# Optimization experiments

Hardware: AMD Instinct MI355X
Metric: run time of the kernel (lower is better)

## Reference

```python
import jax, jax.numpy as jnp
import numpy as np

N = 50000          # nodes
E = 800000         # directed edges (before self-loops)
F_IN = 256
HIDS = 32
HEADS = 8
N_CLASSES = 40
NEG_SLOPE = 0.2    # PyG GATConv default leaky_relu slope


def setup_inputs() -> dict:
    key = jax.random.key(0)
    ks = jax.random.split(key, 10)
    x = jax.random.normal(ks[0], (N, F_IN), dtype=jnp.float32)
    edge_index = jax.random.randint(ks[1], (2, E), 0, N, dtype=jnp.int32)
    # conv1: F_IN -> HIDS per head, HEADS heads, concat=True
    W1 = jax.random.normal(ks[2], (F_IN, HEADS * HIDS), dtype=jnp.float32) * (1.0 / np.sqrt(F_IN))
    a1_src = jax.random.normal(ks[3], (HEADS, HIDS), dtype=jnp.float32) * 0.1
    a1_dst = jax.random.normal(ks[4], (HEADS, HIDS), dtype=jnp.float32) * 0.1
    b1 = jnp.zeros((HEADS * HIDS,), dtype=jnp.float32)
    # conv2: HEADS*HIDS -> N_CLASSES, 1 head, concat=False
    W2 = jax.random.normal(ks[5], (HEADS * HIDS, N_CLASSES), dtype=jnp.float32) * (1.0 / np.sqrt(HEADS * HIDS))
    a2_src = jax.random.normal(ks[6], (1, N_CLASSES), dtype=jnp.float32) * 0.1
    a2_dst = jax.random.normal(ks[7], (1, N_CLASSES), dtype=jnp.float32) * 0.1
    b2 = jnp.zeros((N_CLASSES,), dtype=jnp.float32)
    return {"x": x, "edge_index": edge_index, "W1": W1, "a1_src": a1_src,
            "a1_dst": a1_dst, "b1": b1, "W2": W2, "a2_src": a2_src,
            "a2_dst": a2_dst, "b2": b2}


def _gat_conv(x, src, dst, W, a_src, a_dst, bias, heads, concat):
    n = x.shape[0]
    c = W.shape[1] // heads
    xw = (x @ W).reshape(n, heads, c)                       # [N,H,C]
    alpha_s = jnp.einsum('nhc,hc->nh', xw, a_src)           # [N,H]
    alpha_d = jnp.einsum('nhc,hc->nh', xw, a_dst)
    e = alpha_s[src] + alpha_d[dst]                         # [Etot,H]
    e = jnp.where(e >= 0, e, NEG_SLOPE * e)                 # leaky_relu
    # segment softmax over incoming edges of each destination node
    m = jax.ops.segment_max(e, dst, num_segments=n)         # [N,H]
    ex = jnp.exp(e - m[dst])
    denom = jax.ops.segment_sum(ex, dst, num_segments=n)    # [N,H]
    alpha = ex / denom[dst]                                 # [Etot,H]
    out = jax.ops.segment_sum(alpha[:, :, None] * xw[src], dst, num_segments=n)  # [N,H,C]
    if concat:
        out = out.reshape(n, heads * c)
    else:
        out = out.mean(axis=1)
    return out + bias


def reference(x, edge_index, W1, a1_src, a1_dst, b1, W2, a2_src, a2_dst, b2):
    n = x.shape[0]
    # add self-loops (PyG GATConv default)
    loop = jnp.arange(n, dtype=edge_index.dtype)
    src = jnp.concatenate([edge_index[0], loop])
    dst = jnp.concatenate([edge_index[1], loop])
    # dropout(p=0.6) layers are identity in eval mode
    h = _gat_conv(x, src, dst, W1, a1_src, a1_dst, b1, HEADS, True)
    h = jax.nn.elu(h)
    out = _gat_conv(h, src, dst, W2, a2_src, a2_dst, b2, 1, False)
    return out
```

## Files before the change

kernel.cpp:

```cpp
#include <hip/hip_runtime.h>
#include <hip/hip_bf16.h>

#define NNODES 50000
#define NPAD   50048
#define NEDGES 800000
#define ETOT   (NEDGES + NNODES)
#define FIN    256
#define HIDS   32
#define HEADS  8
#define NCLS   40
#define NEG    0.2f

#define SCAN_B 256
#define NSCB   ((NNODES + SCAN_B - 1) / SCAN_B)

typedef __attribute__((ext_vector_type(8))) short bf16x8;
typedef __attribute__((ext_vector_type(4))) float f32x4;

__device__ __forceinline__ ushort f2bf(float f) {
  unsigned u = __float_as_uint(f);
  unsigned r = (u + 0x7fffu + ((u >> 16) & 1u)) >> 16;
  return (ushort)r;
}
__device__ __forceinline__ float bf2f(ushort u) {
  return __uint_as_float(((unsigned)u) << 16);
}

__global__ __launch_bounds__(256) void conv_x(const float* __restrict__ x, ushort* __restrict__ xb) {
  size_t gid = (size_t)blockIdx.x * 256 + threadIdx.x;
  int row = (int)(gid >> 5);
  int c0 = ((int)gid & 31) * 8;
  if (row >= NPAD) return;
  bf16x8 o;
  if (row < NNODES) {
    const float4* xp = (const float4*)(x + (size_t)row * 256 + c0);
    float4 a = xp[0], b = xp[1];
    o[0] = (short)f2bf(a.x); o[1] = (short)f2bf(a.y);
    o[2] = (short)f2bf(a.z); o[3] = (short)f2bf(a.w);
    o[4] = (short)f2bf(b.x); o[5] = (short)f2bf(b.y);
    o[6] = (short)f2bf(b.z); o[7] = (short)f2bf(b.w);
  } else {
    o = (bf16x8)0;
  }
  *(bf16x8*)(xb + (size_t)row * 256 + c0) = o;
}

__global__ __launch_bounds__(256) void conv_w1t(const float* __restrict__ W1, ushort* __restrict__ w1t) {
  int k = blockIdx.x, n = threadIdx.x;
  w1t[(size_t)n * 256 + k] = f2bf(W1[(size_t)k * 256 + n]);
}

__global__ __launch_bounds__(256) void gemm1_mfma(
    const ushort* __restrict__ xb, const ushort* __restrict__ w1t, ushort* __restrict__ xw1b) {
  __shared__ ushort As[64 * 40];
  __shared__ ushort Bs[256 * 40];
  const int tid = threadIdx.x;
  const int m0 = blockIdx.x * 64;
  const int w = tid >> 6, l = tid & 63, lr = l & 15, lq = l >> 4;
  f32x4 acc[4][4];
#pragma unroll
  for (int i = 0; i < 4; ++i)
#pragma unroll
    for (int j = 0; j < 4; ++j) acc[i][j] = (f32x4)0.f;

  for (int k0 = 0; k0 < 256; k0 += 32) {
    {
      int row = tid >> 2, kg = (tid & 3) * 8;
      *(bf16x8*)&As[row * 40 + kg] = *(const bf16x8*)(xb + (size_t)(m0 + row) * 256 + k0 + kg);
    }
#pragma unroll
    for (int p = 0; p < 4; ++p) {
      int idx = tid + p * 256;
      int n = idx >> 2, kg = (idx & 3) * 8;
      *(bf16x8*)&Bs[n * 40 + kg] = *(const bf16x8*)(w1t + (size_t)n * 256 + k0 + kg);
    }
    __syncthreads();
    bf16x8 af[4], bf[4];
#pragma unroll
    for (int mt = 0; mt < 4; ++mt)
      af[mt] = *(const bf16x8*)&As[(mt * 16 + lr) * 40 + lq * 8];
#pragma unroll
    for (int nt = 0; nt < 4; ++nt)
      bf[nt] = *(const bf16x8*)&Bs[((w * 4 + nt) * 16 + lr) * 40 + lq * 8];
#pragma unroll
    for (int mt = 0; mt < 4; ++mt)
#pragma unroll
      for (int nt = 0; nt < 4; ++nt)
        acc[mt][nt] = __builtin_amdgcn_mfma_f32_16x16x32_bf16(af[mt], bf[nt], acc[mt][nt], 0, 0, 0);
    __syncthreads();
  }
#pragma unroll
  for (int mt = 0; mt < 4; ++mt)
#pragma unroll
    for (int nt = 0; nt < 4; ++nt)
#pragma unroll
      for (int r = 0; r < 4; ++r) {
        int row = m0 + mt * 16 + lq * 4 + r;
        int col = (w * 4 + nt) * 16 + lr;
        xw1b[(size_t)row * 256 + col] = f2bf(acc[mt][nt][r]);
      }
}

#define BM 128
#define BN 64
#define BK 16

__global__ __launch_bounds__(256) void gemm_tiled(
    const float* __restrict__ A, const float* __restrict__ B, float* __restrict__ C,
    int M, int N, int K) {
  __shared__ float As[BK][BM];
  __shared__ float Bs[BK][BN];
  const int tid = threadIdx.x;
  const int tx = tid & 15, ty = tid >> 4;
  const int m0 = blockIdx.x * BM, n0 = blockIdx.y * BN;
  float acc[8][4];
#pragma unroll
  for (int i = 0; i < 8; ++i)
#pragma unroll
    for (int j = 0; j < 4; ++j) acc[i][j] = 0.f;

  for (int k0 = 0; k0 < K; k0 += BK) {
#pragma unroll
    for (int l = 0; l < 2; ++l) {
      int idx = tid + l * 256;
      int r = idx & 127, kg = idx >> 7;
      float4 v = make_float4(0.f, 0.f, 0.f, 0.f);
      int gr = m0 + r;
      if (gr < M) v = *reinterpret_cast<const float4*>(A + (size_t)gr * K + k0 + kg * 4);
      As[kg * 4 + 0][r] = v.x;
      As[kg * 4 + 1][r] = v.y;
      As[kg * 4 + 2][r] = v.z;
      As[kg * 4 + 3][r] = v.w;
    }
    {
      int k = tid >> 4, cg = tid & 15;
      int gc = n0 + cg * 4;
      float4 v = make_float4(0.f, 0.f, 0.f, 0.f);
      if (gc + 3 < N) v = *reinterpret_cast<const float4*>(B + (size_t)(k0 + k) * N + gc);
      *reinterpret_cast<float4*>(&Bs[k][cg * 4]) = v;
    }
    __syncthreads();
#pragma unroll
    for (int k = 0; k < BK; ++k) {
      float4 a0 = *reinterpret_cast<const float4*>(&As[k][ty * 8]);
      float4 a1 = *reinterpret_cast<const float4*>(&As[k][ty * 8 + 4]);
      float4 b  = *reinterpret_cast<const float4*>(&Bs[k][tx * 4]);
      float av[8] = {a0.x, a0.y, a0.z, a0.w, a1.x, a1.y, a1.z, a1.w};
      float bv[4] = {b.x, b.y, b.z, b.w};
#pragma unroll
      for (int i = 0; i < 8; ++i)
#pragma unroll
        for (int j = 0; j < 4; ++j) acc[i][j] += av[i] * bv[j];
    }
    __syncthreads();
  }
#pragma unroll
  for (int i = 0; i < 8; ++i) {
    int gr = m0 + ty * 8 + i;
    if (gr >= M) continue;
    int gc = n0 + tx * 4;
    if (gc + 3 < N) {
      float4 o = make_float4(acc[i][0], acc[i][1], acc[i][2], acc[i][3]);
      *reinterpret_cast<float4*>(C + (size_t)gr * N + gc) = o;
    }
  }
}

__global__ __launch_bounds__(256) void alpha1_k(
    const ushort* __restrict__ xw1b, const float* __restrict__ a1src,
    const float* __restrict__ a1dst, float* __restrict__ os, float* __restrict__ od, int n) {
  int wid = (blockIdx.x * 256 + threadIdx.x) >> 6;
  if (wid >= n) return;
  int lane = threadIdx.x & 63;
  ushort4 u = *(const ushort4*)(xw1b + (size_t)wid * 256 + lane * 4);
  float4 xv = make_float4(bf2f(u.x), bf2f(u.y), bf2f(u.z), bf2f(u.w));
  float4 as = *reinterpret_cast<const float4*>(a1src + lane * 4);
  float4 ad = *reinterpret_cast<const float4*>(a1dst + lane * 4);
  float s = xv.x * as.x + xv.y * as.y + xv.z * as.z + xv.w * as.w;
  float d = xv.x * ad.x + xv.y * ad.y + xv.z * ad.z + xv.w * ad.w;
#pragma unroll
  for (int off = 1; off < 8; off <<= 1) {
    s += __shfl_xor(s, off, 64);
    d += __shfl_xor(d, off, 64);
  }
  if ((lane & 7) == 0) {
    os[(size_t)wid * 8 + (lane >> 3)] = s;
    od[(size_t)wid * 8 + (lane >> 3)] = d;
  }
}

__global__ __launch_bounds__(256) void hist_k(const int* __restrict__ dstA, int* __restrict__ cnt) {
  int e = blockIdx.x * 256 + threadIdx.x;
  if (e >= ETOT) return;
  int d = (e < NEDGES) ? dstA[e] : (e - NEDGES);
  atomicAdd(&cnt[d], 1);
}

__global__ __launch_bounds__(SCAN_B) void scan1_k(const int* __restrict__ deg,
                                                  int* __restrict__ row_ptr,
                                                  int* __restrict__ bsum) {
  __shared__ int sm[SCAN_B];
  int b = blockIdx.x, t = threadIdx.x;
  int idx = b * SCAN_B + t;
  int v = (idx < NNODES) ? deg[idx] : 0;
  sm[t] = v;
  __syncthreads();
#pragma unroll
  for (int off = 1; off < SCAN_B; off <<= 1) {
    int u = (t >= off) ? sm[t - off] : 0;
    __syncthreads();
    sm[t] += u;
    __syncthreads();
  }
  if (idx < NNODES) row_ptr[idx + 1] = sm[t];
  if (t == SCAN_B - 1) bsum[b] = sm[t];
}

__global__ __launch_bounds__(256) void scan2_k(int* __restrict__ bsum) {
  __shared__ int sm[256];
  int t = threadIdx.x;
  sm[t] = (t < NSCB) ? bsum[t] : 0;
  __syncthreads();
#pragma unroll
  for (int off = 1; off < 256; off <<= 1) {
    int u = (t >= off) ? sm[t - off] : 0;
    __syncthreads();
    sm[t] += u;
    __syncthreads();
  }
  if (t < NSCB) bsum[t] = (t > 0) ? sm[t - 1] : 0;
}

__global__ __launch_bounds__(SCAN_B) void scan3_k(const int* __restrict__ bsum,
                                                  int* __restrict__ row_ptr) {
  int b = blockIdx.x, t = threadIdx.x;
  int idx = b * SCAN_B + t;
  if (idx < NNODES) row_ptr[idx + 1] += bsum[b];
  if (b == 0 && t == 0) row_ptr[0] = 0;
}

__global__ __launch_bounds__(256) void scatter_k(const int* __restrict__ srcA, const int* __restrict__ dstA,
                                                 const int* __restrict__ row_ptr, int* __restrict__ cnt,
                                                 int* __restrict__ col) {
  int e = blockIdx.x * 256 + threadIdx.x;
  if (e >= ETOT) return;
  int s, d;
  if (e < NEDGES) { s = srcA[e]; d = dstA[e]; }
  else { s = d = e - NEDGES; }
  int pos = row_ptr[d] + atomicAdd(&cnt[d], 1);
  col[pos] = s;
}

__global__ __launch_bounds__(256) void agg1_k(
    const ushort* __restrict__ xw1b, const float* __restrict__ a1s, const float* __restrict__ a1d,
    const int* __restrict__ row_ptr, const int* __restrict__ col,
    const float* __restrict__ b1, float* __restrict__ hout, int n) {
  int wid = (blockIdx.x * 256 + threadIdx.x) >> 6;
  if (wid >= n) return;
  int lane = threadIdx.x & 63;
  int hh = lane >> 3;
  int beg = row_ptr[wid], end = row_ptr[wid + 1];
  float ad = a1d[(size_t)wid * 8 + hh];
  float denom = 0.f, ax = 0.f, ay = 0.f, az = 0.f, aw = 0.f;
  int i = beg;
  for (; i + 4 <= end; i += 4) {
    int s0 = col[i], s1 = col[i + 1], s2 = col[i + 2], s3 = col[i + 3];
    float e0 = a1s[(size_t)s0 * 8 + hh] + ad;
    float e1 = a1s[(size_t)s1 * 8 + hh] + ad;
    float e2 = a1s[(size_t)s2 * 8 + hh] + ad;
    float e3 = a1s[(size_t)s3 * 8 + hh] + ad;
    ushort4 u0 = *(const ushort4*)(xw1b + (size_t)s0 * 256 + lane * 4);
    ushort4 u1 = *(const ushort4*)(xw1b + (size_t)s1 * 256 + lane * 4);
    ushort4 u2 = *(const ushort4*)(xw1b + (size_t)s2 * 256 + lane * 4);
    ushort4 u3 = *(const ushort4*)(xw1b + (size_t)s3 * 256 + lane * 4);
    float w0 = __expf(fmaxf(e0, 0.f) + NEG * fminf(e0, 0.f));
    float w1 = __expf(fmaxf(e1, 0.f) + NEG * fminf(e1, 0.f));
    float w2 = __expf(fmaxf(e2, 0.f) + NEG * fminf(e2, 0.f));
    float w3 = __expf(fmaxf(e3, 0.f) + NEG * fminf(e3, 0.f));
    denom += (w0 + w1) + (w2 + w3);
    ax += w0 * bf2f(u0.x) + w1 * bf2f(u1.x) + w2 * bf2f(u2.x) + w3 * bf2f(u3.x);
    ay += w0 * bf2f(u0.y) + w1 * bf2f(u1.y) + w2 * bf2f(u2.y) + w3 * bf2f(u3.y);
    az += w0 * bf2f(u0.z) + w1 * bf2f(u1.z) + w2 * bf2f(u2.z) + w3 * bf2f(u3.z);
    aw += w0 * bf2f(u0.w) + w1 * bf2f(u1.w) + w2 * bf2f(u2.w) + w3 * bf2f(u3.w);
  }
  for (; i < end; ++i) {
    int s = col[i];
    float e = a1s[(size_t)s * 8 + hh] + ad;
    float w = __expf(fmaxf(e, 0.f) + NEG * fminf(e, 0.f));
    ushort4 u = *(const ushort4*)(xw1b + (size_t)s * 256 + lane * 4);
    denom += w;
    ax += w * bf2f(u.x); ay += w * bf2f(u.y); az += w * bf2f(u.z); aw += w * bf2f(u.w);
  }
  float inv = 1.f / denom;
  float4 bv = *reinterpret_cast<const float4*>(b1 + lane * 4);
  float ox = ax * inv + bv.x;
  float oy = ay * inv + bv.y;
  float oz = az * inv + bv.z;
  float ow = aw * inv + bv.w;
  ox = (ox > 0.f) ? ox : expm1f(ox);
  oy = (oy > 0.f) ? oy : expm1f(oy);
  oz = (oz > 0.f) ? oz : expm1f(oz);
  ow = (ow > 0.f) ? ow : expm1f(ow);
  *reinterpret_cast<float4*>(hout + (size_t)wid * 256 + lane * 4) =
      make_float4(ox, oy, oz, ow);
}

__global__ __launch_bounds__(256) void alpha2_k(
    const float* __restrict__ xw2, const float* __restrict__ a2s_in, const float* __restrict__ a2d_in,
    float* __restrict__ os, float* __restrict__ od, int n) {
  int v = blockIdx.x * 256 + threadIdx.x;
  if (v >= n) return;
  float s = 0.f, d = 0.f;
#pragma unroll
  for (int j = 0; j < 10; ++j) {
    float4 xv = *reinterpret_cast<const float4*>(xw2 + (size_t)v * 40 + j * 4);
    float4 as = *reinterpret_cast<const float4*>(a2s_in + j * 4);
    float4 ad = *reinterpret_cast<const float4*>(a2d_in + j * 4);
    s += xv.x * as.x + xv.y * as.y + xv.z * as.z + xv.w * as.w;
    d += xv.x * ad.x + xv.y * ad.y + xv.z * ad.z + xv.w * ad.w;
  }
  os[v] = s;
  od[v] = d;
}

__global__ __launch_bounds__(256) void agg2_k(
    const float* __restrict__ xw2, const float* __restrict__ a2s, const float* __restrict__ a2d,
    const int* __restrict__ row_ptr, const int* __restrict__ col,
    const float* __restrict__ b2, float* __restrict__ out, int n) {
  int wid = (blockIdx.x * 256 + threadIdx.x) >> 6;
  if (wid >= n) return;
  int lane = threadIdx.x & 63;
  int beg = row_ptr[wid], end = row_ptr[wid + 1];
  float ad = a2d[wid];
  float denom = 0.f, acc = 0.f;
  int i = beg;
  for (; i + 4 <= end; i += 4) {
    int s0 = col[i], s1 = col[i + 1], s2 = col[i + 2], s3 = col[i + 3];
    float e0 = a2s[s0] + ad;
    float e1 = a2s[s1] + ad;
    float e2 = a2s[s2] + ad;
    float e3 = a2s[s3] + ad;
    float w0 = __expf(fmaxf(e0, 0.f) + NEG * fminf(e0, 0.f));
    float w1 = __expf(fmaxf(e1, 0.f) + NEG * fminf(e1, 0.f));
    float w2 = __expf(fmaxf(e2, 0.f) + NEG * fminf(e2, 0.f));
    float w3 = __expf(fmaxf(e3, 0.f) + NEG * fminf(e3, 0.f));
    float x0 = 0.f, x1 = 0.f, x2 = 0.f, x3 = 0.f;
    if (lane < 40) {
      x0 = xw2[(size_t)s0 * 40 + lane];
      x1 = xw2[(size_t)s1 * 40 + lane];
      x2 = xw2[(size_t)s2 * 40 + lane];
      x3 = xw2[(size_t)s3 * 40 + lane];
    }
    denom += (w0 + w1) + (w2 + w3);
    acc += w0 * x0 + w1 * x1 + w2 * x2 + w3 * x3;
  }
  for (; i < end; ++i) {
    int s = col[i];
    float e = a2s[s] + ad;
    float w = __expf(fmaxf(e, 0.f) + NEG * fminf(e, 0.f));
    denom += w;
    if (lane < 40) acc += w * xw2[(size_t)s * 40 + lane];
  }
  if (lane < 40) out[(size_t)wid * 40 + lane] = acc / denom + b2[lane];
}

extern "C" void kernel_launch(void* const* d_in, const int* in_sizes, int n_in,
                              void* d_out, int out_size, void* d_ws, size_t ws_size,
                              hipStream_t stream) {
  const float* x     = (const float*)d_in[0];
  const int*   ei    = (const int*)d_in[1];
  const float* W1    = (const float*)d_in[2];
  const float* a1src = (const float*)d_in[3];
  const float* a1dst = (const float*)d_in[4];
  const float* b1    = (const float*)d_in[5];
  const float* W2    = (const float*)d_in[6];
  const float* a2src = (const float*)d_in[7];
  const float* a2dst = (const float*)d_in[8];
  const float* b2    = (const float*)d_in[9];
  float* out = (float*)d_out;

  const int* srcA = ei;
  const int* dstA = ei + NEDGES;

  ushort* xb   = (ushort*)d_ws;
  ushort* w1t  = xb + (size_t)NPAD * 256;
  ushort* xw1b = w1t + 65536;
  float*  h    = (float*)(xw1b + (size_t)NPAD * 256);
  float*  a1s  = h + (size_t)NNODES * 256;
  float*  a1d  = a1s + (size_t)NNODES * 8;
  int* ip      = (int*)(a1d + (size_t)NNODES * 8);
  int* row_ptr = ip;
  int* cnt     = ip + (NNODES + 1);
  int* col     = cnt + NNODES;
  int* bsum    = col + ETOT;
  float* xw2 = (float*)xb;
  float* a2s = xw2 + (size_t)NNODES * 40;
  float* a2d = a2s + NNODES;

  hipMemsetAsync(cnt, 0, (size_t)NNODES * sizeof(int), stream);

  conv_x<<<(NPAD * 32) / 256, 256, 0, stream>>>(x, xb);
  conv_w1t<<<256, 256, 0, stream>>>(W1, w1t);
  gemm1_mfma<<<NPAD / 64, 256, 0, stream>>>(xb, w1t, xw1b);

  alpha1_k<<<(NNODES + 3) / 4, 256, 0, stream>>>(xw1b, a1src, a1dst, a1s, a1d, NNODES);

  hist_k<<<(ETOT + 255) / 256, 256, 0, stream>>>(dstA, cnt);
  scan1_k<<<NSCB, SCAN_B, 0, stream>>>(cnt, row_ptr, bsum);
  scan2_k<<<1, 256, 0, stream>>>(bsum);
  scan3_k<<<NSCB, SCAN_B, 0, stream>>>(bsum, row_ptr);
  hipMemsetAsync(cnt, 0, (size_t)NNODES * sizeof(int), stream);
  scatter_k<<<(ETOT + 255) / 256, 256, 0, stream>>>(srcA, dstA, row_ptr, cnt, col);

  agg1_k<<<(NNODES + 3) / 4, 256, 0, stream>>>(xw1b, a1s, a1d, row_ptr, col, b1, h, NNODES);

  {
    dim3 grid((NNODES + BM - 1) / BM, 1);
    gemm_tiled<<<grid, 256, 0, stream>>>(h, W2, xw2, NNODES, NCLS, HEADS * HIDS);
  }

  alpha2_k<<<(NNODES + 255) / 256, 256, 0, stream>>>(xw2, a2src, a2dst, a2s, a2d, NNODES);

  agg2_k<<<(NNODES + 3) / 4, 256, 0, stream>>>(xw2, a2s, a2d, row_ptr, col, b2, out, NNODES);
}
```

Before: 302.8 us.

## Use bf16 MFMA for second GEMM, store h and xw2 in bf16, fuse prep kernels

Replaces the fp32 tiled GEMM for layer 2 with a bf16 MFMA kernel that reads a bf16 copy of the hidden activations and a transposed, zero-padded W2. agg1 now writes h in bf16, and xw2 is kept in bf16, which roughly halves gather traffic in agg2 and alpha2. Input conversion, W1/W2 transposes, zeroing of the counter array and zeroing of the h padding rows are merged into one prep kernel. Both memsets are removed: scatter now uses atomicSub to count down from the histogram values left in cnt. The cost is extra bf16 rounding error in layer 2.

After: 267.4 us. 11.7% less time.

```diff
diff --git a/kernel.cpp b/kernel.cpp
--- a/kernel.cpp
+++ b/kernel.cpp
@@ -14,6 +14,12 @@
 #define SCAN_B 256
 #define NSCB   ((NNODES + SCAN_B - 1) / SCAN_B)
 
+#define PB_X    (NPAD * 32 / 256)
+#define PB_W1   256
+#define PB_W2   64
+#define PB_CNT  ((NNODES + 255) / 256)
+#define PB_HPAD ((NPAD - NNODES))
+
 typedef __attribute__((ext_vector_type(8))) short bf16x8;
 typedef __attribute__((ext_vector_type(4))) float f32x4;
 
@@ -26,28 +32,43 @@
   return __uint_as_float(((unsigned)u) << 16);
 }
 
-__global__ __launch_bounds__(256) void conv_x(const float* __restrict__ x, ushort* __restrict__ xb) {
-  size_t gid = (size_t)blockIdx.x * 256 + threadIdx.x;
-  int row = (int)(gid >> 5);
-  int c0 = ((int)gid & 31) * 8;
-  if (row >= NPAD) return;
-  bf16x8 o;
-  if (row < NNODES) {
-    const float4* xp = (const float4*)(x + (size_t)row * 256 + c0);
-    float4 a = xp[0], b = xp[1];
-    o[0] = (short)f2bf(a.x); o[1] = (short)f2bf(a.y);
-    o[2] = (short)f2bf(a.z); o[3] = (short)f2bf(a.w);
-    o[4] = (short)f2bf(b.x); o[5] = (short)f2bf(b.y);
-    o[6] = (short)f2bf(b.z); o[7] = (short)f2bf(b.w);
+__global__ __launch_bounds__(256) void prep_k(
+    const float* __restrict__ x, const float* __restrict__ W1, const float* __restrict__ W2,
+    ushort* __restrict__ xb, ushort* __restrict__ w1t, ushort* __restrict__ w2t,
+    int* __restrict__ cnt, ushort* __restrict__ hb) {
+  int b = blockIdx.x, t = threadIdx.x;
+  if (b < PB_X) {
+    size_t gid = (size_t)b * 256 + t;
+    int row = (int)(gid >> 5);
+    int c0 = ((int)gid & 31) * 8;
+    bf16x8 o;
+    if (row < NNODES) {
+      const float4* xp = (const float4*)(x + (size_t)row * 256 + c0);
+      float4 a = xp[0], bb = xp[1];
+      o[0] = (short)f2bf(a.x); o[1] = (short)f2bf(a.y);
+      o[2] = (short)f2bf(a.z); o[3] = (short)f2bf(a.w);
+      o[4] = (short)f2bf(bb.x); o[5] = (short)f2bf(bb.y);
+      o[6] = (short)f2bf(bb.z); o[7] = (short)f2bf(bb.w);
+    } else {
+      o = (bf16x8)0;
+    }
+    *(bf16x8*)(xb + (size_t)row * 256 + c0) = o;
+  } else if (b < PB_X + PB_W1) {
+    int idx = (b - PB_X) * 256 + t;
+    int k = idx >> 8, n = idx & 255;
+    w1t[(size_t)n * 256 + k] = f2bf(W1[(size_t)k * 256 + n]);
+  } else if (b < PB_X + PB_W1 + PB_W2) {
+    int idx = (b - PB_X - PB_W1) * 256 + t;
+    int n = idx >> 8, k = idx & 255;
+    w2t[(size_t)n * 256 + k] = (n < NCLS) ? f2bf(W2[(size_t)k * NCLS + n]) : (ushort)0;
+  } else if (b < PB_X + PB_W1 + PB_W2 + PB_CNT) {
+    int i = (b - PB_X - PB_W1 - PB_W2) * 256 + t;
+    if (i < NNODES) cnt[i] = 0;
   } else {
-    o = (bf16x8)0;
-  }
-  *(bf16x8*)(xb + (size_t)row * 256 + c0) = o;
-}
-
-__global__ __launch_bounds__(256) void conv_w1t(const float* __restrict__ W1, ushort* __restrict__ w1t) {
-  int k = blockIdx.x, n = threadIdx.x;
-  w1t[(size_t)n * 256 + k] = f2bf(W1[(size_t)k * 256 + n]);
+    int idx = (b - PB_X - PB_W1 - PB_W2 - PB_CNT);
+    int row = NNODES + idx;
+    hb[(size_t)row * 256 + t] = 0;
+  }
 }
 
 __global__ __launch_bounds__(256) void gemm1_mfma(
@@ -101,67 +122,33 @@
       }
 }
 
-#define BM 128
-#define BN 64
-#define BK 16
-
-__global__ __launch_bounds__(256) void gemm_tiled(
-    const float* __restrict__ A, const float* __restrict__ B, float* __restrict__ C,
-    int M, int N, int K) {
-  __shared__ float As[BK][BM];
-  __shared__ float Bs[BK][BN];
+__global__ __launch_bounds__(256) void gemm2_mfma(
+    const ushort* __restrict__ hb, const ushort* __restrict__ w2t, ushort* __restrict__ xw2b) {
   const int tid = threadIdx.x;
-  const int tx = tid & 15, ty = tid >> 4;
-  const int m0 = blockIdx.x * BM, n0 = blockIdx.y * BN;
-  float acc[8][4];
-#pragma unroll
-  for (int i = 0; i < 8; ++i)
-#pragma unroll
-    for (int j = 0; j < 4; ++j) acc[i][j] = 0.f;
-
-  for (int k0 = 0; k0 < K; k0 += BK) {
-#pragma unroll
-    for (int l = 0; l < 2; ++l) {
-      int idx = tid + l * 256;
-      int r = idx & 127, kg = idx >> 7;
-      float4 v = make_float4(0.f, 0.f, 0.f, 0.f);
-      int gr = m0 + r;
-      if (gr < M) v = *reinterpret_cast<const float4*>(A + (size_t)gr * K + k0 + kg * 4);
-      As[kg * 4 + 0][r] = v.x;
-      As[kg * 4 + 1][r] = v.y;
-      As[kg * 4 + 2][r] = v.z;
-      As[kg * 4 + 3][r] = v.w;
-    }
-    {
-      int k = tid >> 4, cg = tid & 15;
-      int gc = n0 + cg * 4;
-      float4 v = make_float4(0.f, 0.f, 0.f, 0.f);
-      if (gc + 3 < N) v = *reinterpret_cast<const float4*>(B + (size_t)(k0 + k) * N + gc);
-      *reinterpret_cast<float4*>(&Bs[k][cg * 4]) = v;
-    }
-    __syncthreads();
-#pragma unroll
-    for (int k = 0; k < BK; ++k) {
-      float4 a0 = *reinterpret_cast<const float4*>(&As[k][ty * 8]);
-      float4 a1 = *reinterpret_cast<const float4*>(&As[k][ty * 8 + 4]);
-      float4 b  = *reinterpret_cast<const float4*>(&Bs[k][tx * 4]);
-      float av[8] = {a0.x, a0.y, a0.z, a0.w, a1.x, a1.y, a1.z, a1.w};
-      float bv[4] = {b.x, b.y, b.z, b.w};
-#pragma unroll
-      for (int i = 0; i < 8; ++i)
-#pragma unroll
-        for (int j = 0; j < 4; ++j) acc[i][j] += av[i] * bv[j];
-    }
-    __syncthreads();
-  }
-#pragma unroll
-  for (int i = 0; i < 8; ++i) {
-    int gr = m0 + ty * 8 + i;
-    if (gr >= M) continue;
-    int gc = n0 + tx * 4;
-    if (gc + 3 < N) {
-      float4 o = make_float4(acc[i][0], acc[i][1], acc[i][2], acc[i][3]);
-      *reinterpret_cast<float4*>(C + (size_t)gr * N + gc) = o;
+  const int w = tid >> 6, l = tid & 63, lr = l & 15, lq = l >> 4;
+  const int row0 = blockIdx.x * 64 + w * 16;
+  f32x4 acc[4];
+#pragma unroll
+  for (int i = 0; i < 4; ++i) acc[i] = (f32x4)0.f;
+#pragma unroll
+  for (int ks = 0; ks < 8; ++ks) {
+    int k0 = ks * 32;
+    bf16x8 af = *(const bf16x8*)(hb + (size_t)(row0 + lr) * 256 + k0 + lq * 8);
+#pragma unroll
+    for (int nt = 0; nt < 4; ++nt) {
+      bf16x8 bfr = *(const bf16x8*)(w2t + (size_t)(nt * 16 + lr) * 256 + k0 + lq * 8);
+      acc[nt] = __builtin_amdgcn_mfma_f32_16x16x32_bf16(af, bfr, acc[nt], 0, 0, 0);
+    }
+  }
+#pragma unroll
+  for (int nt = 0; nt < 4; ++nt) {
+    int col = nt * 16 + lr;
+    if (col < NCLS) {
+#pragma unroll
+      for (int r = 0; r < 4; ++r) {
+        int row = row0 + lq * 4 + r;
+        xw2b[(size_t)row * 40 + col] = f2bf(acc[nt][r]);
+      }
     }
   }
 }
@@ -247,14 +234,14 @@
   int s, d;
   if (e < NEDGES) { s = srcA[e]; d = dstA[e]; }
   else { s = d = e - NEDGES; }
-  int pos = row_ptr[d] + atomicAdd(&cnt[d], 1);
-  col[pos] = s;
+  int old = atomicSub(&cnt[d], 1);
+  col[row_ptr[d] + old - 1] = s;
 }
 
 __global__ __launch_bounds__(256) void agg1_k(
     const ushort* __restrict__ xw1b, const float* __restrict__ a1s, const float* __restrict__ a1d,
     const int* __restrict__ row_ptr, const int* __restrict__ col,
-    const float* __restrict__ b1, float* __restrict__ hout, int n) {
+    const float* __restrict__ b1, ushort* __restrict__ hb, int n) {
   int wid = (blockIdx.x * 256 + threadIdx.x) >> 6;
   if (wid >= n) return;
   int lane = threadIdx.x & 63;
@@ -301,30 +288,32 @@
   oy = (oy > 0.f) ? oy : expm1f(oy);
   oz = (oz > 0.f) ? oz : expm1f(oz);
   ow = (ow > 0.f) ? ow : expm1f(ow);
-  *reinterpret_cast<float4*>(hout + (size_t)wid * 256 + lane * 4) =
-      make_float4(ox, oy, oz, ow);
+  ushort4 ho;
+  ho.x = f2bf(ox); ho.y = f2bf(oy); ho.z = f2bf(oz); ho.w = f2bf(ow);
+  *(ushort4*)(hb + (size_t)wid * 256 + lane * 4) = ho;
 }
 
 __global__ __launch_bounds__(256) void alpha2_k(
-    const float* __restrict__ xw2, const float* __restrict__ a2s_in, const float* __restrict__ a2d_in,
+    const ushort* __restrict__ xw2b, const float* __restrict__ a2s_in, const float* __restrict__ a2d_in,
     float* __restrict__ os, float* __restrict__ od, int n) {
   int v = blockIdx.x * 256 + threadIdx.x;
   if (v >= n) return;
+  const ushort* row = xw2b + (size_t)v * 40;
   float s = 0.f, d = 0.f;
 #pragma unroll
   for (int j = 0; j < 10; ++j) {
-    float4 xv = *reinterpret_cast<const float4*>(xw2 + (size_t)v * 40 + j * 4);
+    ushort4 u = *(const ushort4*)(row + j * 4);
     float4 as = *reinterpret_cast<const float4*>(a2s_in + j * 4);
     float4 ad = *reinterpret_cast<const float4*>(a2d_in + j * 4);
-    s += xv.x * as.x + xv.y * as.y + xv.z * as.z + xv.w * as.w;
-    d += xv.x * ad.x + xv.y * ad.y + xv.z * ad.z + xv.w * ad.w;
+    s += bf2f(u.x) * as.x + bf2f(u.y) * as.y + bf2f(u.z) * as.z + bf2f(u.w) * as.w;
+    d += bf2f(u.x) * ad.x + bf2f(u.y) * ad.y + bf2f(u.z) * ad.z + bf2f(u.w) * ad.w;
   }
   os[v] = s;
   od[v] = d;
 }
 
 __global__ __launch_bounds__(256) void agg2_k(
-    const float* __restrict__ xw2, const float* __restrict__ a2s, const float* __restrict__ a2d,
+    const ushort* __restrict__ xw2b, const float* __restrict__ a2s, const float* __restrict__ a2d,
     const int* __restrict__ row_ptr, const int* __restrict__ col,
     const float* __restrict__ b2, float* __restrict__ out, int n) {
   int wid = (blockIdx.x * 256 + threadIdx.x) >> 6;
@@ -345,11 +334,11 @@
     float w2 = __expf(fmaxf(e2, 0.f) + NEG * fminf(e2, 0.f));
     float w3 = __expf(fmaxf(e3, 0.f) + NEG * fminf(e3, 0.f));
     float x0 = 0.f, x1 = 0.f, x2 = 0.f, x3 = 0.f;
-    if (lane < 40) {
-      x0 = xw2[(size_t)s0 * 40 + lane];
-      x1 = xw2[(size_t)s1 * 40 + lane];
-      x2 = xw2[(size_t)s2 * 40 + lane];
-      x3 = xw2[(size_t)s3 * 40 + lane];
+    if (lane < NCLS) {
+      x0 = bf2f(xw2b[(size_t)s0 * 40 + lane]);
+      x1 = bf2f(xw2b[(size_t)s1 * 40 + lane]);
+      x2 = bf2f(xw2b[(size_t)s2 * 40 + lane]);
+      x3 = bf2f(xw2b[(size_t)s3 * 40 + lane]);
     }
     denom += (w0 + w1) + (w2 + w3);
     acc += w0 * x0 + w1 * x1 + w2 * x2 + w3 * x3;
@@ -359,9 +348,9 @@
     float e = a2s[s] + ad;
     float w = __expf(fmaxf(e, 0.f) + NEG * fminf(e, 0.f));
     denom += w;
-    if (lane < 40) acc += w * xw2[(size_t)s * 40 + lane];
-  }
-  if (lane < 40) out[(size_t)wid * 40 + lane] = acc / denom + b2[lane];
+    if (lane < NCLS) acc += w * bf2f(xw2b[(size_t)s * 40 + lane]);
+  }
+  if (lane < NCLS) out[(size_t)wid * 40 + lane] = acc / denom + b2[lane];
 }
 
 extern "C" void kernel_launch(void* const* d_in, const int* in_sizes, int n_in,
@@ -384,23 +373,22 @@
 
   ushort* xb   = (ushort*)d_ws;
   ushort* w1t  = xb + (size_t)NPAD * 256;
-  ushort* xw1b = w1t + 65536;
-  float*  h    = (float*)(xw1b + (size_t)NPAD * 256);
-  float*  a1s  = h + (size_t)NNODES * 256;
-  float*  a1d  = a1s + (size_t)NNODES * 8;
-  int* ip      = (int*)(a1d + (size_t)NNODES * 8);
-  int* row_ptr = ip;
-  int* cnt     = ip + (NNODES + 1);
+  ushort* w2t  = w1t + 65536;
+  ushort* xw1b = w2t + 16384;
+  ushort* hb   = xw1b + (size_t)NPAD * 256;
+  ushort* xw2b = hb + (size_t)NPAD * 256;
+  float* a1s   = (float*)(xw2b + (size_t)NPAD * 40);
+  float* a1d   = a1s + (size_t)NNODES * 8;
+  float* a2s   = a1d + (size_t)NNODES * 8;
+  float* a2d   = a2s + NNODES;
+  int* row_ptr = (int*)(a2d + NNODES);
+  int* cnt     = row_ptr + (NNODES + 1);
   int* col     = cnt + NNODES;
   int* bsum    = col + ETOT;
-  float* xw2 = (float*)xb;
-  float* a2s = xw2 + (size_t)NNODES * 40;
-  float* a2d = a2s + NNODES;
-
-  hipMemsetAsync(cnt, 0, (size_t)NNODES * sizeof(int), stream);
-
-  conv_x<<<(NPAD * 32) / 256, 256, 0, stream>>>(x, xb);
-  conv_w1t<<<256, 256, 0, stream>>>(W1, w1t);
+
+  prep_k<<<PB_X + PB_W1 + PB_W2 + PB_CNT + PB_HPAD, 256, 0, stream>>>(
+      x, W1, W2, xb, w1t, w2t, cnt, hb);
+
   gemm1_mfma<<<NPAD / 64, 256, 0, stream>>>(xb, w1t, xw1b);
 
   alpha1_k<<<(NNODES + 3) / 4, 256, 0, stream>>>(xw1b, a1src, a1dst, a1s, a1d, NNODES);
@@ -409,17 +397,13 @@
   scan1_k<<<NSCB, SCAN_B, 0, stream>>>(cnt, row_ptr, bsum);
   scan2_k<<<1, 256, 0, stream>>>(bsum);
   scan3_k<<<NSCB, SCAN_B, 0, stream>>>(bsum, row_ptr);
-  hipMemsetAsync(cnt, 0, (size_t)NNODES * sizeof(int), stream);
   scatter_k<<<(ETOT + 255) / 256, 256, 0, stream>>>(srcA, dstA, row_ptr, cnt, col);
 
-  agg1_k<<<(NNODES + 3) / 4, 256, 0, stream>>>(xw1b, a1s, a1d, row_ptr, col, b1, h, NNODES);
-
-  {
-    dim3 grid((NNODES + BM - 1) / BM, 1);
-    gemm_tiled<<<grid, 256, 0, stream>>>(h, W2, xw2, NNODES, NCLS, HEADS * HIDS);
-  }
-
-  alpha2_k<<<(NNODES + 255) / 256, 256, 0, stream>>>(xw2, a2src, a2dst, a2s, a2d, NNODES);
-
-  agg2_k<<<(NNODES + 3) / 4, 256, 0, stream>>>(xw2, a2s, a2d, row_ptr, col, b2, out, NNODES);
-}
+  agg1_k<<<(NNODES + 3) / 4, 256, 0, stream>>>(xw1b, a1s, a1d, row_ptr, col, b1, hb, NNODES);
+
+  gemm2_mfma<<<NPAD / 64, 256, 0, stream>>>(hb, w2t, xw2b);
+
+  alpha2_k<<<(NNODES + 255) / 256, 256, 0, stream>>>(xw2b, a2src, a2dst, a2s, a2d, NNODES);
+
+  agg2_k<<<(NNODES + 3) / 4, 256, 0, stream>>>(xw2b, a2s, a2d, row_ptr, col, b2, out, NNODES);
+}
```
